# Kernel tuning notes

Hardware: AMD Instinct MI355X
Metric: run time of the kernel (lower is better)

## Reference

```python
import math
import jax, jax.numpy as jnp
import numpy as np

N_EMBD = 1024
N_HEAD = 16
B, T = 2, 2048
MASK_VALUE = -1000000.0


def setup_inputs() -> dict:
    key = jax.random.key(0)
    ks = jax.random.split(key, 10)
    s = 1.0 / math.sqrt(N_EMBD)
    x = jax.random.normal(ks[0], (B, T, N_EMBD), dtype=jnp.float32)
    # torch.nn.Linear weights are (out_features, in_features)
    Wq = jax.random.normal(ks[1], (N_EMBD, N_EMBD), dtype=jnp.float32) * s
    bq = jax.random.normal(ks[2], (N_EMBD,), dtype=jnp.float32) * s
    Wk = jax.random.normal(ks[3], (N_EMBD, N_EMBD), dtype=jnp.float32) * s
    bk = jax.random.normal(ks[4], (N_EMBD,), dtype=jnp.float32) * s
    Wv = jax.random.normal(ks[5], (N_EMBD, N_EMBD), dtype=jnp.float32) * s
    bv = jax.random.normal(ks[6], (N_EMBD,), dtype=jnp.float32) * s
    Wp = jax.random.normal(ks[7], (N_EMBD, N_EMBD), dtype=jnp.float32) * s
    bp = jax.random.normal(ks[8], (N_EMBD,), dtype=jnp.float32) * s
    # causal attn mask (B, T, T): 1 where attention allowed
    attn_mask = jnp.broadcast_to(
        jnp.tril(jnp.ones((T, T), dtype=jnp.int32))[None], (B, T, T))
    valid_input_mask = jnp.ones((B, T), dtype=jnp.int32)
    return {"x": x, "Wq": Wq, "bq": bq, "Wk": Wk, "bk": bk,
            "Wv": Wv, "bv": bv, "Wp": Wp, "bp": bp,
            "attn_mask": attn_mask, "valid_input_mask": valid_input_mask}


def reference(x, Wq, bq, Wk, bk, Wv, bv, Wp, bp, attn_mask, valid_input_mask):
    Bb, Tt, C = x.shape
    H = N_HEAD
    d = C // H
    # projections (torch Linear: x @ W.T + b), split into heads -> (B, H, T, d)
    def heads(y):
        return y.reshape(Bb, Tt, H, d).transpose(0, 2, 1, 3)
    q = heads(x @ Wq.T + bq)
    k = heads(x @ Wk.T + bk)
    v = heads(x @ Wv.T + bv)
    # attention scores (B, H, T, T)
    att = jnp.einsum('bhtd,bhsd->bhts', q, k) * (1.0 / math.sqrt(d))
    att = jnp.where(attn_mask[:, None, :, :] == 0, MASK_VALUE, att)
    att = jnp.where(valid_input_mask[:, None, None, :] == 0, MASK_VALUE, att)
    att = jax.nn.softmax(att, axis=-1)
    y = jnp.einsum('bhts,bhsd->bhtd', att, v)
    y = y.transpose(0, 2, 1, 3).reshape(Bb, Tt, C)
    return y @ Wp.T + bp
```

## Files before the change

kernel.cpp:

```cpp
#include <hip/hip_runtime.h>
#include <hip/hip_bf16.h>
#include <stdint.h>

typedef unsigned short u16;
typedef __attribute__((ext_vector_type(8))) short bf16x8;
typedef __attribute__((ext_vector_type(4))) float f32x4;

#define AS1 __attribute__((address_space(1)))
#define AS3 __attribute__((address_space(3)))

__device__ __forceinline__ void gload_lds16(const void* g, void* l) {
  __builtin_amdgcn_global_load_lds((const AS1 void*)g, (AS3 void*)l, 16, 0, 0);
}

__device__ __forceinline__ u16 f2bf(float f) {
  union { float f; uint32_t u; } v; v.f = f;
  uint32_t r = v.u + 0x7FFFu + ((v.u >> 16) & 1u);
  return (u16)(r >> 16);
}

__global__ void cvt_all(const float* __restrict__ x,
                        const float* __restrict__ w0, const float* __restrict__ w1,
                        const float* __restrict__ w2, const float* __restrict__ w3,
                        u16* __restrict__ x16, u16* __restrict__ w16) {
  int i = blockIdx.x * 256 + threadIdx.x;
  const float* src; u16* dst; int off;
  if (i < 1048576) { src = x; dst = x16; off = i; }
  else {
    int j = i - 1048576; int w = j >> 18; off = j & 262143;
    src = (w == 0) ? w0 : (w == 1) ? w1 : (w == 2) ? w2 : w3;
    dst = w16 + (size_t)w * 1048576;
  }
  float4 v = ((const float4*)src)[off];
  uint64_t pk = (uint64_t)f2bf(v.x) | ((uint64_t)f2bf(v.y) << 16) |
                ((uint64_t)f2bf(v.z) << 32) | ((uint64_t)f2bf(v.w) << 48);
  ((uint64_t*)dst)[off] = pk;
}

#define BM 128
#define BN 128
#define BK 32

template<int MODE>
__global__ __launch_bounds__(256, 2)
void gemm_bt(const u16* __restrict__ A, const u16* __restrict__ Bw,
             const float* __restrict__ bias0, const float* __restrict__ bias1,
             const float* __restrict__ bias2, void* __restrict__ Out,
             int M, int N, int K)
{
  __shared__ __align__(16) u16 As[BM * BK];
  __shared__ __align__(16) u16 Bs[BN * BK];
  const int tid = threadIdx.x;
  const int lane = tid & 63, wid = tid >> 6;
  const int lr = lane & 15, lg = lane >> 4;
  const int m0 = blockIdx.y * BM, n0 = blockIdx.x * BN;
  const int z = blockIdx.z;
  const u16* Bz = Bw + (size_t)z * N * K;
  const float* bias = (MODE == 0) ? (z == 0 ? bias0 : (z == 1 ? bias1 : bias2)) : bias0;
  const int wm = (wid >> 1) * 64, wn = (wid & 1) * 64;

  f32x4 acc[4][4] = {};

  for (int kt = 0; kt < K; kt += BK) {
    __syncthreads();
#pragma unroll
    for (int i = 0; i < 2; ++i) {
      int cb = (i * 4 + wid) * 64;
      int c = cb + lane;
      int row = c >> 2, kc = (c & 3) * 8;
      gload_lds16(A  + (size_t)(m0 + row) * K + kt + kc, (void*)&As[(size_t)cb * 8]);
      gload_lds16(Bz + (size_t)(n0 + row) * K + kt + kc, (void*)&Bs[(size_t)cb * 8]);
    }
    __syncthreads();

    bf16x8 af[4], bfr[4];
#pragma unroll
    for (int mf = 0; mf < 4; ++mf) af[mf]  = *(const bf16x8*)&As[(wm + mf * 16 + lr) * BK + lg * 8];
#pragma unroll
    for (int nf = 0; nf < 4; ++nf) bfr[nf] = *(const bf16x8*)&Bs[(wn + nf * 16 + lr) * BK + lg * 8];
#pragma unroll
    for (int mf = 0; mf < 4; ++mf)
#pragma unroll
      for (int nf = 0; nf < 4; ++nf)
        acc[mf][nf] = __builtin_amdgcn_mfma_f32_16x16x32_bf16(af[mf], bfr[nf], acc[mf][nf], 0, 0, 0);
  }

#pragma unroll
  for (int nf = 0; nf < 4; ++nf) {
    float bv = bias[n0 + wn + nf * 16 + lr];
#pragma unroll
    for (int mf = 0; mf < 4; ++mf)
#pragma unroll
      for (int r = 0; r < 4; ++r) {
        int m = m0 + wm + mf * 16 + lg * 4 + r;
        int n = n0 + wn + nf * 16 + lr;
        float v = acc[mf][nf][r] + bv;
        if (MODE == 0) {
          if (z == 0) v *= 0.125f;
          size_t addr = ((size_t)(m >> 11) * 16 + (n >> 6)) * (size_t)(2048 * 64)
                      + (size_t)(m & 2047) * 64 + (n & 63);
          ((u16*)Out)[(size_t)z * 4194304 + addr] = f2bf(v);
        } else {
          ((float*)Out)[(size_t)m * N + n] = v;
        }
      }
  }
}

__global__ void transpose_v(const u16* __restrict__ v, u16* __restrict__ vt) {
  __shared__ __align__(16) u16 t[64][72];
  const int tid = threadIdx.x;
  const int s0 = blockIdx.x * 64;
  const int bh = blockIdx.y;
  const u16* src = v + (size_t)bh * 2048 * 64;
  u16* dst = vt + (size_t)bh * 64 * 2048;
#pragma unroll
  for (int i = 0; i < 2; ++i) {
    int c = tid + i * 256;
    int r = c >> 3, col = (c & 7) * 8;
    *(bf16x8*)&t[r][col] = *(const bf16x8*)&src[(size_t)(s0 + r) * 64 + col];
  }
  __syncthreads();
#pragma unroll
  for (int i = 0; i < 2; ++i) {
    int c = tid + i * 256;
    int d = c >> 3, sc = (c & 7) * 8;
    bf16x8 o;
#pragma unroll
    for (int j = 0; j < 8; ++j) o[j] = (short)t[sc + j][d];
    *(bf16x8*)&dst[(size_t)d * 2048 + s0 + sc] = o;
  }
}

__global__ __launch_bounds__(256, 4)
void attn_fwd(const u16* __restrict__ q, const u16* __restrict__ k,
              const u16* __restrict__ vt, u16* __restrict__ y)
{
  __shared__ __align__(16) u16 Ks[64 * 64];
  __shared__ __align__(16) u16 Vs[64 * 64];
  __shared__ __align__(16) u16 Ps[4][16 * 72];
  const int tid = threadIdx.x, lane = tid & 63, wid = tid >> 6;
  const int lr = lane & 15, lg = lane >> 4;
  const int qt = 31 - ((blockIdx.x + blockIdx.y) & 31);
  const int q0 = qt * 64;
  const int bh = blockIdx.y;
  const u16* qg = q + (size_t)bh * 2048 * 64;
  const u16* kg = k + (size_t)bh * 2048 * 64;
  const u16* vg = vt + (size_t)bh * 64 * 2048;
  const int trow0 = q0 + wid * 16;

  bf16x8 qa[2];
#pragma unroll
  for (int kk = 0; kk < 2; ++kk)
    qa[kk] = *(const bf16x8*)&qg[(size_t)(trow0 + lr) * 64 + kk * 32 + lg * 8];

  const int l8 = lane >> 3, s8 = lane & 7;
  const int r0 = wid * 16 + l8;
  const u16* kld = kg + (size_t)r0 * 64 + s8 * 8;
  const u16* vld = vg + (size_t)r0 * 2048 + s8 * 8;
  u16* kst0 = &Ks[r0 * 64 + (s8 ^ l8) * 8];
  u16* kst1 = &Ks[(r0 + 8) * 64 + (s8 ^ l8) * 8];
  u16* vst0 = &Vs[r0 * 64 + (s8 ^ l8) * 8];
  u16* vst1 = &Vs[(r0 + 8) * 64 + (s8 ^ l8) * 8];

  bf16x8 ldK0, ldK1, ldV0, ldV1;
  ldK0 = *(const bf16x8*)(kld);
  ldK1 = *(const bf16x8*)(kld + 8 * 64);
  ldV0 = *(const bf16x8*)(vld);
  ldV1 = *(const bf16x8*)(vld + 8 * 2048);

  f32x4 oacc[4] = {};
  float mrun = -1e30f, lrun = 0.f;
  const int nkt = qt + 1;
  const int xsl = lr & 7;
  const int tq = trow0 + lr;

  for (int kt = 0; kt < nkt; ++kt) {
    *(bf16x8*)kst0 = ldK0;  *(bf16x8*)kst1 = ldK1;
    *(bf16x8*)vst0 = ldV0;  *(bf16x8*)vst1 = ldV1;
    if (kt + 1 < nkt) {
      const u16* kn = kld + (size_t)(kt + 1) * 4096;
      const u16* vn = vld + (size_t)(kt + 1) * 64;
      ldK0 = *(const bf16x8*)(kn);
      ldK1 = *(const bf16x8*)(kn + 8 * 64);
      ldV0 = *(const bf16x8*)(vn);
      ldV1 = *(const bf16x8*)(vn + 8 * 2048);
    }
    asm volatile("s_waitcnt lgkmcnt(0)" ::: "memory");
    __builtin_amdgcn_s_barrier();

    f32x4 sacc[4] = {};
#pragma unroll
    for (int kk = 0; kk < 2; ++kk) {
      bf16x8 kb[4];
#pragma unroll
      for (int sf = 0; sf < 4; ++sf)
        kb[sf] = *(const bf16x8*)&Ks[(sf * 16 + lr) * 64 + (((kk * 4 + lg) ^ xsl) * 8)];
#pragma unroll
      for (int sf = 0; sf < 4; ++sf)
        sacc[sf] = __builtin_amdgcn_mfma_f32_16x16x32_bf16(kb[sf], qa[kk], sacc[sf], 0, 0, 0);
    }

    if (kt == qt) {
#pragma unroll
      for (int sf = 0; sf < 4; ++sf)
#pragma unroll
        for (int r = 0; r < 4; ++r) {
          int s = kt * 64 + sf * 16 + lg * 4 + r;
          if (s > tq) sacc[sf][r] = -1e30f;
        }
    }

    float mx = -1e30f;
#pragma unroll
    for (int sf = 0; sf < 4; ++sf)
#pragma unroll
      for (int r = 0; r < 4; ++r) mx = fmaxf(mx, sacc[sf][r]);
    mx = fmaxf(mx, __shfl_xor(mx, 16));
    mx = fmaxf(mx, __shfl_xor(mx, 32));
    if (!__all(mx - mrun <= 8.0f)) {
      float mn = fmaxf(mrun, mx);
      float scn = __expf(mrun - mn);
      mrun = mn;
      lrun *= scn;
      float scr[4];
#pragma unroll
      for (int r = 0; r < 4; ++r) scr[r] = __shfl(scn, lg * 4 + r);
#pragma unroll
      for (int nf = 0; nf < 4; ++nf)
#pragma unroll
        for (int r = 0; r < 4; ++r) oacc[nf][r] *= scr[r];
    }
    float rs = 0.f;
#pragma unroll
    for (int sf = 0; sf < 4; ++sf)
#pragma unroll
      for (int r = 0; r < 4; ++r) {
        float p = __expf(sacc[sf][r] - mrun);
        sacc[sf][r] = p;
        rs += p;
      }
    rs += __shfl_xor(rs, 16);
    rs += __shfl_xor(rs, 32);
    lrun += rs;

#pragma unroll
    for (int sf = 0; sf < 4; ++sf) {
      union { ushort4 u; uint2 d; } pk_;
      pk_.u.x = f2bf(sacc[sf][0]); pk_.u.y = f2bf(sacc[sf][1]);
      pk_.u.z = f2bf(sacc[sf][2]); pk_.u.w = f2bf(sacc[sf][3]);
      *(uint2*)&Ps[wid][lr * 72 + sf * 16 + lg * 4] = pk_.d;
    }

#pragma unroll
    for (int kk = 0; kk < 2; ++kk) {
      bf16x8 pa, vb[4];
      pa = *(const bf16x8*)&Ps[wid][lr * 72 + kk * 32 + lg * 8];
#pragma unroll
      for (int nf = 0; nf < 4; ++nf)
        vb[nf] = *(const bf16x8*)&Vs[(nf * 16 + lr) * 64 + (((kk * 4 + lg) ^ xsl) * 8)];
#pragma unroll
      for (int nf = 0; nf < 4; ++nf)
        oacc[nf] = __builtin_amdgcn_mfma_f32_16x16x32_bf16(pa, vb[nf], oacc[nf], 0, 0, 0);
    }

    asm volatile("s_waitcnt lgkmcnt(0)" ::: "memory");
    __builtin_amdgcn_s_barrier();
  }

  const int b = bh >> 4, h = bh & 15;
#pragma unroll
  for (int r = 0; r < 4; ++r) {
    float lshf = __shfl(lrun, lg * 4 + r);
    float inv = 1.f / lshf;
    int t = trow0 + lg * 4 + r;
#pragma unroll
    for (int nf = 0; nf < 4; ++nf) {
      int n = nf * 16 + lr;
      y[((size_t)b * 2048 + t) * 1024 + h * 64 + n] = f2bf(oacc[nf][r] * inv);
    }
  }
}

extern "C" void kernel_launch(void* const* d_in, const int* in_sizes, int n_in,
                              void* d_out, int out_size, void* d_ws, size_t ws_size,
                              hipStream_t stream) {
  const float* x  = (const float*)d_in[0];
  const float* Wq = (const float*)d_in[1];
  const float* bq = (const float*)d_in[2];
  const float* Wk = (const float*)d_in[3];
  const float* bk = (const float*)d_in[4];
  const float* Wv = (const float*)d_in[5];
  const float* bv = (const float*)d_in[6];
  const float* Wp = (const float*)d_in[7];
  const float* bp = (const float*)d_in[8];

  char* ws = (char*)d_ws;
  u16* x16  = (u16*)(ws + (size_t)0);
  u16* w16  = (u16*)(ws + ((size_t)8  << 20));
  u16* q16  = (u16*)(ws + ((size_t)16 << 20));
  u16* k16  = (u16*)(ws + ((size_t)24 << 20));
  u16* v16  = (u16*)(ws + ((size_t)32 << 20));
  u16* vt16 = (u16*)(ws + ((size_t)40 << 20));
  u16* y16  = x16;

  cvt_all<<<8192, 256, 0, stream>>>(x, Wq, Wk, Wv, Wp, x16, w16);
  gemm_bt<0><<<dim3(8, 32, 3), 256, 0, stream>>>(x16, w16, bq, bk, bv, (void*)q16, 4096, 1024, 1024);
  transpose_v<<<dim3(32, 32), 256, 0, stream>>>(v16, vt16);
  attn_fwd<<<dim3(32, 32), 256, 0, stream>>>(q16, k16, vt16, y16);
  gemm_bt<1><<<dim3(8, 32, 1), 256, 0, stream>>>(y16, w16 + 3 * 1048576, bp, bp, bp, d_out, 4096, 1024, 1024);
}
```

Before: 126.6 us.

## Enlarge attention tiles to 128 queries and 128 keys with 512-thread blocks

The attention kernel now uses 8 waves per block, covering 128 query rows, and loads 128-key K/V tiles into LDS per iteration, with the V LDS layout and swizzle changed to 128-wide rows. Each K/V tile is shared across twice as many query rows, and there are half as many barrier-synchronised iterations. The causal tile order is also changed so that the two halves of the bh range run in opposite orders, to balance load. In exchange, the larger LDS footprint and 512-thread blocks may lower occupancy, the grid has fewer blocks, and the diagonal tile wastes more masked work.

New measurement: 120.8 us. 4.5% less time.

```diff
diff --git a/kernel.cpp b/kernel.cpp
--- a/kernel.cpp
+++ b/kernel.cpp
@@ -132,22 +132,25 @@
   }
 }
 
-__global__ __launch_bounds__(256, 4)
+__global__ __launch_bounds__(512, 4)
 void attn_fwd(const u16* __restrict__ q, const u16* __restrict__ k,
               const u16* __restrict__ vt, u16* __restrict__ y)
 {
-  __shared__ __align__(16) u16 Ks[64 * 64];
-  __shared__ __align__(16) u16 Vs[64 * 64];
-  __shared__ __align__(16) u16 Ps[4][16 * 72];
+  __shared__ __align__(16) u16 Ks[128 * 64];
+  __shared__ __align__(16) u16 Vs[64 * 128];
+  __shared__ __align__(16) u16 Ps[8][16 * 136];
   const int tid = threadIdx.x, lane = tid & 63, wid = tid >> 6;
   const int lr = lane & 15, lg = lane >> 4;
-  const int qt = 31 - ((blockIdx.x + blockIdx.y) & 31);
-  const int q0 = qt * 64;
-  const int bh = blockIdx.y;
+  const int bx = blockIdx.x, by = blockIdx.y;
+  const int r4 = (bx + by) & 15;
+  const int qt = (by & 16) ? r4 : 15 - r4;
+  const int q0 = qt * 128;
+  const int bh = by;
   const u16* qg = q + (size_t)bh * 2048 * 64;
   const u16* kg = k + (size_t)bh * 2048 * 64;
   const u16* vg = vt + (size_t)bh * 64 * 2048;
   const int trow0 = q0 + wid * 16;
+  const int tq = trow0 + lr;
 
   bf16x8 qa[2];
 #pragma unroll
@@ -155,67 +158,71 @@
     qa[kk] = *(const bf16x8*)&qg[(size_t)(trow0 + lr) * 64 + kk * 32 + lg * 8];
 
   const int l8 = lane >> 3, s8 = lane & 7;
-  const int r0 = wid * 16 + l8;
-  const u16* kld = kg + (size_t)r0 * 64 + s8 * 8;
-  const u16* vld = vg + (size_t)r0 * 2048 + s8 * 8;
-  u16* kst0 = &Ks[r0 * 64 + (s8 ^ l8) * 8];
-  u16* kst1 = &Ks[(r0 + 8) * 64 + (s8 ^ l8) * 8];
-  u16* vst0 = &Vs[r0 * 64 + (s8 ^ l8) * 8];
-  u16* vst1 = &Vs[(r0 + 8) * 64 + (s8 ^ l8) * 8];
+  const int kr0 = wid * 16 + l8;
+  const int vd  = wid * 8 + l8;
+  const u16* kld = kg + (size_t)kr0 * 64 + s8 * 8;
+  const u16* vld = vg + (size_t)vd * 2048 + s8 * 8;
+  u16* kst0 = &Ks[kr0 * 64 + (s8 ^ l8) * 8];
+  u16* kst1 = &Ks[(kr0 + 8) * 64 + (s8 ^ l8) * 8];
+  u16* vst0 = &Vs[vd * 128 + ((s8    ) ^ (vd & 7)) * 8];
+  u16* vst1 = &Vs[vd * 128 + ((s8 + 8) ^ (vd & 7)) * 8];
 
   bf16x8 ldK0, ldK1, ldV0, ldV1;
   ldK0 = *(const bf16x8*)(kld);
   ldK1 = *(const bf16x8*)(kld + 8 * 64);
   ldV0 = *(const bf16x8*)(vld);
-  ldV1 = *(const bf16x8*)(vld + 8 * 2048);
+  ldV1 = *(const bf16x8*)(vld + 64);
 
   f32x4 oacc[4] = {};
   float mrun = -1e30f, lrun = 0.f;
-  const int nkt = qt + 1;
+  const int nk2 = qt + 1;
   const int xsl = lr & 7;
-  const int tq = trow0 + lr;
-
-  for (int kt = 0; kt < nkt; ++kt) {
+
+  for (int j = 0; j < nk2; ++j) {
     *(bf16x8*)kst0 = ldK0;  *(bf16x8*)kst1 = ldK1;
     *(bf16x8*)vst0 = ldV0;  *(bf16x8*)vst1 = ldV1;
-    if (kt + 1 < nkt) {
-      const u16* kn = kld + (size_t)(kt + 1) * 4096;
-      const u16* vn = vld + (size_t)(kt + 1) * 64;
+    if (j + 1 < nk2) {
+      const u16* kn = kld + (size_t)(j + 1) * 8192;
+      const u16* vn = vld + (size_t)(j + 1) * 128;
       ldK0 = *(const bf16x8*)(kn);
       ldK1 = *(const bf16x8*)(kn + 8 * 64);
       ldV0 = *(const bf16x8*)(vn);
-      ldV1 = *(const bf16x8*)(vn + 8 * 2048);
+      ldV1 = *(const bf16x8*)(vn + 64);
     }
     asm volatile("s_waitcnt lgkmcnt(0)" ::: "memory");
     __builtin_amdgcn_s_barrier();
 
-    f32x4 sacc[4] = {};
+    f32x4 sacc[8] = {};
 #pragma unroll
     for (int kk = 0; kk < 2; ++kk) {
-      bf16x8 kb[4];
-#pragma unroll
-      for (int sf = 0; sf < 4; ++sf)
+      bf16x8 kb[8];
+#pragma unroll
+      for (int sf = 0; sf < 8; ++sf)
         kb[sf] = *(const bf16x8*)&Ks[(sf * 16 + lr) * 64 + (((kk * 4 + lg) ^ xsl) * 8)];
 #pragma unroll
-      for (int sf = 0; sf < 4; ++sf)
+      for (int sf = 0; sf < 8; ++sf)
         sacc[sf] = __builtin_amdgcn_mfma_f32_16x16x32_bf16(kb[sf], qa[kk], sacc[sf], 0, 0, 0);
     }
 
-    if (kt == qt) {
-#pragma unroll
-      for (int sf = 0; sf < 4; ++sf)
+    if (j == qt) {
+#pragma unroll
+      for (int sf = 0; sf < 8; ++sf)
 #pragma unroll
         for (int r = 0; r < 4; ++r) {
-          int s = kt * 64 + sf * 16 + lg * 4 + r;
+          int s = j * 128 + sf * 16 + lg * 4 + r;
           if (s > tq) sacc[sf][r] = -1e30f;
         }
     }
 
-    float mx = -1e30f;
-#pragma unroll
-    for (int sf = 0; sf < 4; ++sf)
-#pragma unroll
-      for (int r = 0; r < 4; ++r) mx = fmaxf(mx, sacc[sf][r]);
+    float m01 = fmaxf(fmaxf(fmaxf(sacc[0][0], sacc[0][1]), fmaxf(sacc[0][2], sacc[0][3])),
+                      fmaxf(fmaxf(sacc[1][0], sacc[1][1]), fmaxf(sacc[1][2], sacc[1][3])));
+    float m23 = fmaxf(fmaxf(fmaxf(sacc[2][0], sacc[2][1]), fmaxf(sacc[2][2], sacc[2][3])),
+                      fmaxf(fmaxf(sacc[3][0], sacc[3][1]), fmaxf(sacc[3][2], sacc[3][3])));
+    float m45 = fmaxf(fmaxf(fmaxf(sacc[4][0], sacc[4][1]), fmaxf(sacc[4][2], sacc[4][3])),
+                      fmaxf(fmaxf(sacc[5][0], sacc[5][1]), fmaxf(sacc[5][2], sacc[5][3])));
+    float m67 = fmaxf(fmaxf(fmaxf(sacc[6][0], sacc[6][1]), fmaxf(sacc[6][2], sacc[6][3])),
+                      fmaxf(fmaxf(sacc[7][0], sacc[7][1]), fmaxf(sacc[7][2], sacc[7][3])));
+    float mx = fmaxf(fmaxf(m01, m23), fmaxf(m45, m67));
     mx = fmaxf(mx, __shfl_xor(mx, 16));
     mx = fmaxf(mx, __shfl_xor(mx, 32));
     if (!__all(mx - mrun <= 8.0f)) {
@@ -233,7 +240,7 @@
     }
     float rs = 0.f;
 #pragma unroll
-    for (int sf = 0; sf < 4; ++sf)
+    for (int sf = 0; sf < 8; ++sf)
 #pragma unroll
       for (int r = 0; r < 4; ++r) {
         float p = __expf(sacc[sf][r] - mrun);
@@ -245,20 +252,20 @@
     lrun += rs;
 
 #pragma unroll
-    for (int sf = 0; sf < 4; ++sf) {
+    for (int sf = 0; sf < 8; ++sf) {
       union { ushort4 u; uint2 d; } pk_;
       pk_.u.x = f2bf(sacc[sf][0]); pk_.u.y = f2bf(sacc[sf][1]);
       pk_.u.z = f2bf(sacc[sf][2]); pk_.u.w = f2bf(sacc[sf][3]);
-      *(uint2*)&Ps[wid][lr * 72 + sf * 16 + lg * 4] = pk_.d;
-    }
-
-#pragma unroll
-    for (int kk = 0; kk < 2; ++kk) {
-      bf16x8 pa, vb[4];
-      pa = *(const bf16x8*)&Ps[wid][lr * 72 + kk * 32 + lg * 8];
+      *(uint2*)&Ps[wid][lr * 136 + sf * 16 + lg * 4] = pk_.d;
+    }
+
+#pragma unroll
+    for (int kk = 0; kk < 4; ++kk) {
+      bf16x8 pa = *(const bf16x8*)&Ps[wid][lr * 136 + kk * 32 + lg * 8];
+      bf16x8 vb[4];
 #pragma unroll
       for (int nf = 0; nf < 4; ++nf)
-        vb[nf] = *(const bf16x8*)&Vs[(nf * 16 + lr) * 64 + (((kk * 4 + lg) ^ xsl) * 8)];
+        vb[nf] = *(const bf16x8*)&Vs[(nf * 16 + lr) * 128 + (((kk * 4 + lg) ^ xsl) * 8)];
 #pragma unroll
       for (int nf = 0; nf < 4; ++nf)
         oacc[nf] = __builtin_amdgcn_mfma_f32_16x16x32_bf16(pa, vb[nf], oacc[nf], 0, 0, 0);
@@ -307,6 +314,6 @@
   cvt_all<<<8192, 256, 0, stream>>>(x, Wq, Wk, Wv, Wp, x16, w16);
   gemm_bt<0><<<dim3(8, 32, 3), 256, 0, stream>>>(x16, w16, bq, bk, bv, (void*)q16, 4096, 1024, 1024);
   transpose_v<<<dim3(32, 32), 256, 0, stream>>>(v16, vt16);
-  attn_fwd<<<dim3(32, 32), 256, 0, stream>>>(q16, k16, vt16, y16);
+  attn_fwd<<<dim3(16, 32), 512, 0, stream>>>(q16, k16, vt16, y16);
   gemm_bt<1><<<dim3(8, 32, 1), 256, 0, stream>>>(y16, w16 + 3 * 1048576, bp, bp, bp, d_out, 4096, 1024, 1024);
 }
```

## Use 128-row query tiles with 8 waves in attention and exp2-based softmax

Applied to the files above, without the earlier changes.

The attention kernel now processes 128 query rows per block with 8 waves (512 threads), so each K/V tile loaded to LDS is shared across twice as many query rows. Waves whose rows are fully masked for a given K tile skip the compute but still take part in the barriers. The Q scale now folds in log2(e), so softmax can use exp2f, and the rescale threshold is adjusted to match. Conversions use packed bf16 intrinsics. The trade-offs are idle waves on the diagonal tiles and a different block schedule.

New measurement: 156.3 us. 23.5% more time.

```diff
diff --git a/kernel.cpp b/kernel.cpp
--- a/kernel.cpp
+++ b/kernel.cpp
@@ -32,9 +32,10 @@
     dst = w16 + (size_t)w * 1048576;
   }
   float4 v = ((const float4*)src)[off];
-  uint64_t pk = (uint64_t)f2bf(v.x) | ((uint64_t)f2bf(v.y) << 16) |
-                ((uint64_t)f2bf(v.z) << 32) | ((uint64_t)f2bf(v.w) << 48);
-  ((uint64_t*)dst)[off] = pk;
+  union { __hip_bfloat162 h[2]; uint64_t u; } o;
+  o.h[0] = __float22bfloat162_rn(float2{v.x, v.y});
+  o.h[1] = __float22bfloat162_rn(float2{v.z, v.w});
+  ((uint64_t*)dst)[off] = o.u;
 }
 
 #define BM 128
@@ -96,7 +97,7 @@
         int n = n0 + wn + nf * 16 + lr;
         float v = acc[mf][nf][r] + bv;
         if (MODE == 0) {
-          if (z == 0) v *= 0.125f;
+          if (z == 0) v *= 0.18033688f;
           size_t addr = ((size_t)(m >> 11) * 16 + (n >> 6)) * (size_t)(2048 * 64)
                       + (size_t)(m & 2047) * 64 + (n & 63);
           ((u16*)Out)[(size_t)z * 4194304 + addr] = f2bf(v);
@@ -132,22 +133,26 @@
   }
 }
 
-__global__ __launch_bounds__(256, 4)
+__global__ __launch_bounds__(512, 8)
 void attn_fwd(const u16* __restrict__ q, const u16* __restrict__ k,
               const u16* __restrict__ vt, u16* __restrict__ y)
 {
   __shared__ __align__(16) u16 Ks[64 * 64];
   __shared__ __align__(16) u16 Vs[64 * 64];
-  __shared__ __align__(16) u16 Ps[4][16 * 72];
+  __shared__ __align__(16) u16 Ps[8][16 * 72];
   const int tid = threadIdx.x, lane = tid & 63, wid = tid >> 6;
   const int lr = lane & 15, lg = lane >> 4;
-  const int qt = 31 - ((blockIdx.x + blockIdx.y) & 31);
-  const int q0 = qt * 64;
-  const int bh = blockIdx.y;
+  const int bx = blockIdx.x, by = blockIdx.y;
+  const int r4 = (bx + by) & 15;
+  const int qt = (by & 16) ? r4 : 15 - r4;
+  const int q0 = qt * 128;
+  const int bh = by;
   const u16* qg = q + (size_t)bh * 2048 * 64;
   const u16* kg = k + (size_t)bh * 2048 * 64;
   const u16* vg = vt + (size_t)bh * 64 * 2048;
   const int trow0 = q0 + wid * 16;
+  const int tq = trow0 + lr;
+  const int dtile = trow0 >> 6;
 
   bf16x8 qa[2];
 #pragma unroll
@@ -155,113 +160,105 @@
     qa[kk] = *(const bf16x8*)&qg[(size_t)(trow0 + lr) * 64 + kk * 32 + lg * 8];
 
   const int l8 = lane >> 3, s8 = lane & 7;
-  const int r0 = wid * 16 + l8;
-  const u16* kld = kg + (size_t)r0 * 64 + s8 * 8;
-  const u16* vld = vg + (size_t)r0 * 2048 + s8 * 8;
-  u16* kst0 = &Ks[r0 * 64 + (s8 ^ l8) * 8];
-  u16* kst1 = &Ks[(r0 + 8) * 64 + (s8 ^ l8) * 8];
-  u16* vst0 = &Vs[r0 * 64 + (s8 ^ l8) * 8];
-  u16* vst1 = &Vs[(r0 + 8) * 64 + (s8 ^ l8) * 8];
-
-  bf16x8 ldK0, ldK1, ldV0, ldV1;
-  ldK0 = *(const bf16x8*)(kld);
-  ldK1 = *(const bf16x8*)(kld + 8 * 64);
-  ldV0 = *(const bf16x8*)(vld);
-  ldV1 = *(const bf16x8*)(vld + 8 * 2048);
+  const int kr = wid * 8 + l8;
+  const u16* kld = kg + (size_t)kr * 64 + s8 * 8;
+  const u16* vld = vg + (size_t)kr * 2048 + s8 * 8;
+  u16* kst = &Ks[kr * 64 + (s8 ^ l8) * 8];
+  u16* vst = &Vs[kr * 64 + (s8 ^ l8) * 8];
+
+  bf16x8 ldK = *(const bf16x8*)kld;
+  bf16x8 ldV = *(const bf16x8*)vld;
 
   f32x4 oacc[4] = {};
   float mrun = -1e30f, lrun = 0.f;
-  const int nkt = qt + 1;
+  const int nkt = 2 * qt + 2;
   const int xsl = lr & 7;
-  const int tq = trow0 + lr;
 
   for (int kt = 0; kt < nkt; ++kt) {
-    *(bf16x8*)kst0 = ldK0;  *(bf16x8*)kst1 = ldK1;
-    *(bf16x8*)vst0 = ldV0;  *(bf16x8*)vst1 = ldV1;
+    *(bf16x8*)kst = ldK;
+    *(bf16x8*)vst = ldV;
     if (kt + 1 < nkt) {
-      const u16* kn = kld + (size_t)(kt + 1) * 4096;
-      const u16* vn = vld + (size_t)(kt + 1) * 64;
-      ldK0 = *(const bf16x8*)(kn);
-      ldK1 = *(const bf16x8*)(kn + 8 * 64);
-      ldV0 = *(const bf16x8*)(vn);
-      ldV1 = *(const bf16x8*)(vn + 8 * 2048);
+      ldK = *(const bf16x8*)(kld + (size_t)(kt + 1) * 4096);
+      ldV = *(const bf16x8*)(vld + (size_t)(kt + 1) * 64);
     }
     asm volatile("s_waitcnt lgkmcnt(0)" ::: "memory");
     __builtin_amdgcn_s_barrier();
 
-    f32x4 sacc[4] = {};
-#pragma unroll
-    for (int kk = 0; kk < 2; ++kk) {
-      bf16x8 kb[4];
+    if (kt <= dtile) {
+      f32x4 sacc[4] = {};
+#pragma unroll
+      for (int kk = 0; kk < 2; ++kk) {
+        bf16x8 kb[4];
+#pragma unroll
+        for (int sf = 0; sf < 4; ++sf)
+          kb[sf] = *(const bf16x8*)&Ks[(sf * 16 + lr) * 64 + (((kk * 4 + lg) ^ xsl) * 8)];
+#pragma unroll
+        for (int sf = 0; sf < 4; ++sf)
+          sacc[sf] = __builtin_amdgcn_mfma_f32_16x16x32_bf16(kb[sf], qa[kk], sacc[sf], 0, 0, 0);
+      }
+
+      if (kt == dtile) {
+#pragma unroll
+        for (int sf = 0; sf < 4; ++sf)
+#pragma unroll
+          for (int r = 0; r < 4; ++r) {
+            int s = kt * 64 + sf * 16 + lg * 4 + r;
+            if (s > tq) sacc[sf][r] = -1e30f;
+          }
+      }
+
+      float mx = -1e30f;
 #pragma unroll
       for (int sf = 0; sf < 4; ++sf)
-        kb[sf] = *(const bf16x8*)&Ks[(sf * 16 + lr) * 64 + (((kk * 4 + lg) ^ xsl) * 8)];
+#pragma unroll
+        for (int r = 0; r < 4; ++r) mx = fmaxf(mx, sacc[sf][r]);
+      mx = fmaxf(mx, __shfl_xor(mx, 16));
+      mx = fmaxf(mx, __shfl_xor(mx, 32));
+      if (!__all(mx - mrun <= 11.5f)) {
+        float mn = fmaxf(mrun, mx);
+        float scn = exp2f(mrun - mn);
+        mrun = mn;
+        lrun *= scn;
+        float scr[4];
+#pragma unroll
+        for (int r = 0; r < 4; ++r) scr[r] = __shfl(scn, lg * 4 + r);
+#pragma unroll
+        for (int nf = 0; nf < 4; ++nf)
+#pragma unroll
+          for (int r = 0; r < 4; ++r) oacc[nf][r] *= scr[r];
+      }
+      float rs = 0.f;
 #pragma unroll
       for (int sf = 0; sf < 4; ++sf)
-        sacc[sf] = __builtin_amdgcn_mfma_f32_16x16x32_bf16(kb[sf], qa[kk], sacc[sf], 0, 0, 0);
-    }
-
-    if (kt == qt) {
-#pragma unroll
-      for (int sf = 0; sf < 4; ++sf)
 #pragma unroll
         for (int r = 0; r < 4; ++r) {
-          int s = kt * 64 + sf * 16 + lg * 4 + r;
-          if (s > tq) sacc[sf][r] = -1e30f;
+          float p = exp2f(sacc[sf][r] - mrun);
+          sacc[sf][r] = p;
+          rs += p;
         }
-    }
-
-    float mx = -1e30f;
-#pragma unroll
-    for (int sf = 0; sf < 4; ++sf)
-#pragma unroll
-      for (int r = 0; r < 4; ++r) mx = fmaxf(mx, sacc[sf][r]);
-    mx = fmaxf(mx, __shfl_xor(mx, 16));
-    mx = fmaxf(mx, __shfl_xor(mx, 32));
-    if (!__all(mx - mrun <= 8.0f)) {
-      float mn = fmaxf(mrun, mx);
-      float scn = __expf(mrun - mn);
-      mrun = mn;
-      lrun *= scn;
-      float scr[4];
-#pragma unroll
-      for (int r = 0; r < 4; ++r) scr[r] = __shfl(scn, lg * 4 + r);
-#pragma unroll
-      for (int nf = 0; nf < 4; ++nf)
-#pragma unroll
-        for (int r = 0; r < 4; ++r) oacc[nf][r] *= scr[r];
-    }
-    float rs = 0.f;
-#pragma unroll
-    for (int sf = 0; sf < 4; ++sf)
-#pragma unroll
-      for (int r = 0; r < 4; ++r) {
-        float p = __expf(sacc[sf][r] - mrun);
-        sacc[sf][r] = p;
-        rs += p;
-      }
-    rs += __shfl_xor(rs, 16);
-    rs += __shfl_xor(rs, 32);
-    lrun += rs;
-
-#pragma unroll
-    for (int sf = 0; sf < 4; ++sf) {
-      union { ushort4 u; uint2 d; } pk_;
-      pk_.u.x = f2bf(sacc[sf][0]); pk_.u.y = f2bf(sacc[sf][1]);
-      pk_.u.z = f2bf(sacc[sf][2]); pk_.u.w = f2bf(sacc[sf][3]);
-      *(uint2*)&Ps[wid][lr * 72 + sf * 16 + lg * 4] = pk_.d;
-    }
-
-#pragma unroll
-    for (int kk = 0; kk < 2; ++kk) {
-      bf16x8 pa, vb[4];
-      pa = *(const bf16x8*)&Ps[wid][lr * 72 + kk * 32 + lg * 8];
-#pragma unroll
-      for (int nf = 0; nf < 4; ++nf)
-        vb[nf] = *(const bf16x8*)&Vs[(nf * 16 + lr) * 64 + (((kk * 4 + lg) ^ xsl) * 8)];
-#pragma unroll
-      for (int nf = 0; nf < 4; ++nf)
-        oacc[nf] = __builtin_amdgcn_mfma_f32_16x16x32_bf16(pa, vb[nf], oacc[nf], 0, 0, 0);
+      rs += __shfl_xor(rs, 16);
+      rs += __shfl_xor(rs, 32);
+      lrun += rs;
+
+#pragma unroll
+      for (int sf = 0; sf < 4; ++sf) {
+        union { __hip_bfloat162 h[2]; uint2 d; } pk_;
+        pk_.h[0] = __float22bfloat162_rn(float2{sacc[sf][0], sacc[sf][1]});
+        pk_.h[1] = __float22bfloat162_rn(float2{sacc[sf][2], sacc[sf][3]});
+        *(uint2*)&Ps[wid][lr * 72 + sf * 16 + lg * 4] = pk_.d;
+      }
+
+#pragma unroll
+      for (int kk = 0; kk < 2; ++kk) {
+        bf16x8 pa = *(const bf16x8*)&Ps[wid][lr * 72 + kk * 32 + lg * 8];
+        bf16x8 vb[4];
+#pragma unroll
+        for (int nf = 0; nf < 4; ++nf)
+          vb[nf] = *(const bf16x8*)&Vs[(nf * 16 + lr) * 64 + (((kk * 4 + lg) ^ xsl) * 8)];
+#pragma unroll
+        for (int nf = 0; nf < 4; ++nf)
+          oacc[nf] = __builtin_amdgcn_mfma_f32_16x16x32_bf16(pa, vb[nf], oacc[nf], 0, 0, 0);
+      }
     }
 
     asm volatile("s_waitcnt lgkmcnt(0)" ::: "memory");
@@ -307,6 +304,6 @@
   cvt_all<<<8192, 256, 0, stream>>>(x, Wq, Wk, Wv, Wp, x16, w16);
   gemm_bt<0><<<dim3(8, 32, 3), 256, 0, stream>>>(x16, w16, bq, bk, bv, (void*)q16, 4096, 1024, 1024);
   transpose_v<<<dim3(32, 32), 256, 0, stream>>>(v16, vt16);
-  attn_fwd<<<dim3(32, 32), 256, 0, stream>>>(q16, k16, vt16, y16);
+  attn_fwd<<<dim3(16, 32), 512, 0, stream>>>(q16, k16, vt16, y16);
   gemm_bt<1><<<dim3(8, 32, 1), 256, 0, stream>>>(y16, w16 + 3 * 1048576, bp, bp, bp, d_out, 4096, 1024, 1024);
 }
```
